# Kernel tuning notes

Measured on AMD Instinct MI355X. Metric: run time of the kernel, lower is better.

Reference implementation:

```python
import jax, jax.numpy as jnp
import numpy as np

EPS = 0.01
BETA = 0.8
GAMMA_A = 0.01
GAMMA_W = 0.01
ALPHA = 1.0
N_UNITS = 128

def setup_inputs() -> dict:
    key = jax.random.key(0)
    ks = jax.random.split(key, 7)
    B, T, D_in, C_out = 512, 1024, 64, 10
    return {
        "x": jax.random.normal(ks[0], (B, T, D_in), dtype=jnp.float32),
        "E_w": jax.random.normal(ks[1], (N_UNITS, D_in), dtype=jnp.float32) / np.sqrt(D_in),
        "E_b": jax.random.normal(ks[2], (N_UNITS,), dtype=jnp.float32) * 0.01,
        "B_p": jax.random.normal(ks[3], (N_UNITS, N_UNITS), dtype=jnp.float32) / N_UNITS,
        "C_p": jax.random.normal(ks[4], (N_UNITS, N_UNITS), dtype=jnp.float32) / N_UNITS,
        "D_w": jax.random.normal(ks[5], (C_out, N_UNITS), dtype=jnp.float32) / np.sqrt(N_UNITS),
        "D_b": jax.random.normal(ks[6], (C_out,), dtype=jnp.float32) * 0.01,
    }

def reference(x, E_w, E_b, B_p, C_p, D_w, D_b):
    B, T, _ = x.shape
    I = jnp.eye(N_UNITS, dtype=x.dtype)
    # Skew/symmetric mixture recurrent matrices (computed once, as in i==0 branch)
    A = BETA * (B_p - B_p.T) + (1.0 - BETA) * (B_p + B_p.T) - GAMMA_A * I
    W = BETA * (C_p - C_p.T) + (1.0 - BETA) * (C_p + C_p.T) - GAMMA_W * I
    # Input projection for all timesteps at once: [T, B, n_units]
    Z = jnp.einsum('bti,ui->tbu', x, E_w) + E_b
    h0 = jnp.zeros((B, N_UNITS), dtype=x.dtype)

    def step(h, z):
        h_update = ALPHA * (h @ A) + jnp.tanh(h @ W + z)
        return h + EPS * h_update, None

    h_final, _ = jax.lax.scan(step, h0, Z)
    return h_final @ D_w.T + D_b
```

## Files before the change

kernel.cpp:

```cpp
#include <hip/hip_runtime.h>

#define EPS_C 0.01f
#define NU    128
#define DIN   64
#define COUT  10

typedef float    f32x4 __attribute__((ext_vector_type(4)));
typedef _Float16 f16x4 __attribute__((ext_vector_type(4)));
typedef _Float16 f16x8 __attribute__((ext_vector_type(8)));

#define MFMA32(A, B, C) __builtin_amdgcn_mfma_f32_16x16x32_f16((A), (B), (C), 0, 0, 0)
#define BAR() asm volatile("s_waitcnt lgkmcnt(0)\n\ts_barrier" ::: "memory")

__global__ __launch_bounds__(256, 1)
void rnn_core(const float* __restrict__ x,
              const float* __restrict__ E_w, const float* __restrict__ E_b,
              const float* __restrict__ B_p, const float* __restrict__ C_p,
              const float* __restrict__ D_w, const float* __restrict__ D_b,
              float* __restrict__ out, int T)
{
    const int tid  = threadIdx.x;
    const int lane = tid & 63;
    const int w    = tid >> 6;
    const int lid  = lane & 15;
    const int q    = lane >> 4;
    const int g    = blockIdx.x;

    __shared__ __attribute__((aligned(16))) _Float16 xs[2][8 * 1024];
    __shared__ __attribute__((aligned(16))) _Float16 hbuf[2][4][64][8];
    __shared__ float hfin[16][NU + 4];

    f16x8 AT[2][4], WT[2][4], EF[2][2];
    f32x4 ebv[2];
    #pragma unroll
    for (int mt = 0; mt < 2; ++mt) {
        const int m = w * 32 + mt * 16 + lid;
        #pragma unroll
        for (int kt = 0; kt < 4; ++kt) {
            f16x8 fa, fw;
            #pragma unroll
            for (int j = 0; j < 8; ++j) {
                const int k  = kt * 32 + q * 8 + j;
                const float dg = (k == m) ? 0.01f : 0.0f;
                fa[j] = (_Float16)(B_p[k * NU + m] - 0.6f * B_p[m * NU + k] - dg);
                fw[j] = (_Float16)(C_p[k * NU + m] - 0.6f * C_p[m * NU + k] - dg);
            }
            AT[mt][kt] = fa;  WT[mt][kt] = fw;
        }
        #pragma unroll
        for (int kt = 0; kt < 2; ++kt) {
            f16x8 fe;
            #pragma unroll
            for (int j = 0; j < 8; ++j)
                fe[j] = (_Float16)E_w[m * DIN + kt * 32 + q * 8 + j];
            EF[mt][kt] = fe;
        }
        #pragma unroll
        for (int r = 0; r < 4; ++r)
            ebv[mt][r] = E_b[w * 32 + mt * 16 + q * 4 + r];
    }

    const int bb = tid & 15;
    const int s2 = tid >> 4;
    const float* xrow = x + ((size_t)(g * 16 + bb) * T) * DIN + s2 * 4;
    const int wb2 = (((s2 >> 3) * 64) + (((s2 >> 1) & 3) * 16) + bb) * 16 + (s2 & 1) * 8;

    float4 xg[8];

#define STAGE_WRITE(BUF)                                                      \
    {                                                                         \
        char* base_ = (char*)&xs[(BUF)][0];                                   \
        _Pragma("unroll")                                                     \
        for (int i2 = 0; i2 < 8; ++i2) {                                      \
            float4 v_ = xg[i2];                                               \
            f16x4 h4_;                                                        \
            h4_[0] = (_Float16)v_.x; h4_[1] = (_Float16)v_.y;                 \
            h4_[2] = (_Float16)v_.z; h4_[3] = (_Float16)v_.w;                 \
            *(f16x4*)(base_ + i2 * 2048 + wb2) = h4_;                         \
        }                                                                     \
    }

    ((float4*)&hbuf[0][0][0][0])[tid] = (float4){0.f, 0.f, 0.f, 0.f};
    #pragma unroll
    for (int i = 0; i < 8; ++i)
        xg[i] = *(const float4*)(xrow + (size_t)i * DIN);
    STAGE_WRITE(0)
    __syncthreads();

    char* xsb = (char*)&xs[0][0] + lane * 16;
    char* hrb = (char*)&hbuf[0][0][0][0] + lane * 16;
    char* hwb = (char*)&hbuf[0][0][0][0]
              + (w * 64 + (q >> 1) * 16 + lid) * 16 + (q & 1) * 8;

    f32x4 hf[2] = {{0.f,0.f,0.f,0.f}, {0.f,0.f,0.f,0.f}};
    f32x4 zc0, zc1;
    {
        f16x8 x0 = *(const f16x8*)(xsb);
        f16x8 x1 = *(const f16x8*)(xsb + 1024);
        zc0 = ebv[0];
        zc0 = MFMA32(EF[0][0], x0, zc0);
        zc0 = MFMA32(EF[0][1], x1, zc0);
        zc1 = ebv[1];
        zc1 = MFMA32(EF[1][0], x0, zc1);
        zc1 = MFMA32(EF[1][1], x1, zc1);
    }

    const int nch = T >> 3;
    for (int c = 0; c < nch; ++c) {
        if (c + 1 < nch) {
            const float* xr2 = xrow + (size_t)(c + 1) * 8 * DIN;
            #pragma unroll
            for (int i = 0; i < 8; ++i)
                xg[i] = *(const float4*)(xr2 + (size_t)i * DIN);
        }
        #pragma unroll
        for (int i = 0; i < 8; ++i) {
            const int t  = c * 8 + i;
            const int p  = i & 1;
            const int np = p ^ 1;

            f16x8 hB[4];
            #pragma unroll
            for (int kt = 0; kt < 4; ++kt)
                hB[kt] = *(const f16x8*)(hrb + p * 4096 + kt * 1024);

            int tt = t + 1; if (tt >= T) tt = T - 1;
            char* xb = xsb + ((tt >> 3) & 1) * 16384 + (tt & 7) * 2048;
            f16x8 xfA = *(const f16x8*)(xb);
            f16x8 xfB = *(const f16x8*)(xb + 1024);

            f32x4 wa0 = zc0, wa1 = zc1;
            #pragma unroll
            for (int kt = 0; kt < 4; ++kt) {
                wa0 = MFMA32(WT[0][kt], hB[kt], wa0);
                wa1 = MFMA32(WT[1][kt], hB[kt], wa1);
            }
            f32x4 ya0 = {0.f,0.f,0.f,0.f}, ya1 = {0.f,0.f,0.f,0.f};
            #pragma unroll
            for (int kt = 0; kt < 4; ++kt) {
                ya0 = MFMA32(AT[0][kt], hB[kt], ya0);
                ya1 = MFMA32(AT[1][kt], hB[kt], ya1);
            }
            f32x4 zn0 = ebv[0], zn1 = ebv[1];
            zn0 = MFMA32(EF[0][0], xfA, zn0);
            zn1 = MFMA32(EF[1][0], xfA, zn1);
            zn0 = MFMA32(EF[0][1], xfB, zn0);
            zn1 = MFMA32(EF[1][1], xfB, zn1);

            #pragma unroll
            for (int mt = 0; mt < 2; ++mt) {
                f32x4 wa = mt ? wa1 : wa0;
                f32x4 ya = mt ? ya1 : ya0;
                f16x4 nh;
                #pragma unroll
                for (int r = 0; r < 4; ++r) {
                    const float e2 = __builtin_amdgcn_exp2f(wa[r] * 2.8853900817779268f);
                    const float th = 1.0f - 2.0f * __builtin_amdgcn_rcpf(e2 + 1.0f);
                    const float hv = hf[mt][r] + EPS_C * (ya[r] + th);
                    hf[mt][r] = hv;
                    nh[r] = (_Float16)hv;
                }
                *(f16x4*)(hwb + np * 4096 + mt * 512) = nh;
            }
            zc0 = zn0; zc1 = zn1;

            if (i == 5 && c + 1 < nch) STAGE_WRITE((c + 1) & 1)
            BAR();
        }
    }

    #pragma unroll
    for (int mt = 0; mt < 2; ++mt)
        #pragma unroll
        for (int r = 0; r < 4; ++r)
            hfin[lid][w * 32 + mt * 16 + q * 4 + r] = hf[mt][r];
    __syncthreads();

    if (tid < 16 * COUT) {
        const int r  = tid / COUT;
        const int cc = tid - r * COUT;
        float acc = D_b[cc];
        #pragma unroll 8
        for (int u = 0; u < NU; ++u)
            acc = fmaf(hfin[r][u], D_w[cc * NU + u], acc);
        out[((size_t)g * 16 + r) * COUT + cc] = acc;
    }
}

extern "C" void kernel_launch(void* const* d_in, const int* in_sizes, int n_in,
                              void* d_out, int out_size, void* d_ws, size_t ws_size,
                              hipStream_t stream)
{
    const float* x   = (const float*)d_in[0];
    const float* E_w = (const float*)d_in[1];
    const float* E_b = (const float*)d_in[2];
    const float* B_p = (const float*)d_in[3];
    const float* C_p = (const float*)d_in[4];
    const float* D_w = (const float*)d_in[5];
    const float* D_b = (const float*)d_in[6];
    float* out = (float*)d_out;

    const int B  = out_size / COUT;
    const int T  = in_sizes[0] / (B * DIN);
    const int NB = B / 16;

    rnn_core<<<NB, 256, 0, stream>>>(x, E_w, E_b, B_p, C_p, D_w, D_b, out, T);
}
```

Before: 588.1 us.

## Process two independent 16-row batch groups per block to interleave recurrence chains

Each block now handles 32 batch rows as two independent groups that share the register-resident recurrent and input-projection weight fragments. The MFMA chains and tanh updates of the two groups are interleaved within each timestep so one group's work can fill the other's latency, and the per-step barrier is shared. The x staging for the second group is spread across different substeps. This halves the grid size, leaving more CUs idle and doubling per-step work and register pressure per block.

```diff
diff --git a/kernel.cpp b/kernel.cpp
--- a/kernel.cpp
+++ b/kernel.cpp
@@ -26,9 +26,9 @@
     const int q    = lane >> 4;
     const int g    = blockIdx.x;
 
-    __shared__ __attribute__((aligned(16))) _Float16 xs[2][8 * 1024];
-    __shared__ __attribute__((aligned(16))) _Float16 hbuf[2][4][64][8];
-    __shared__ float hfin[16][NU + 4];
+    __shared__ __attribute__((aligned(16))) _Float16 xs[2][2][8192];
+    __shared__ __attribute__((aligned(16))) _Float16 hbuf[2][2][4][64][8];
+    __shared__ float hfin[32][NU + 4];
 
     f16x8 AT[2][4], WT[2][4], EF[2][2];
     f32x4 ebv[2];
@@ -62,14 +62,15 @@
 
     const int bb = tid & 15;
     const int s2 = tid >> 4;
-    const float* xrow = x + ((size_t)(g * 16 + bb) * T) * DIN + s2 * 4;
+    const float* xrow0 = x + ((size_t)(g * 32 + bb) * T) * DIN + s2 * 4;
+    const float* xrow1 = xrow0 + (size_t)16 * T * DIN;
     const int wb2 = (((s2 >> 3) * 64) + (((s2 >> 1) & 3) * 16) + bb) * 16 + (s2 & 1) * 8;
 
     float4 xg[8];
 
-#define STAGE_WRITE(BUF)                                                      \
+#define STAGE_WRITE(GR, BUF)                                                  \
     {                                                                         \
-        char* base_ = (char*)&xs[(BUF)][0];                                   \
+        char* base_ = (char*)xs + (GR) * 32768 + (BUF) * 16384;               \
         _Pragma("unroll")                                                     \
         for (int i2 = 0; i2 < 8; ++i2) {                                      \
             float4 v_ = xg[i2];                                               \
@@ -80,110 +81,151 @@
         }                                                                     \
     }
 
-    ((float4*)&hbuf[0][0][0][0])[tid] = (float4){0.f, 0.f, 0.f, 0.f};
+    #pragma unroll
+    for (int k2 = 0; k2 < 4; ++k2)
+        ((float4*)hbuf)[k2 * 256 + tid] = (float4){0.f, 0.f, 0.f, 0.f};
     #pragma unroll
     for (int i = 0; i < 8; ++i)
-        xg[i] = *(const float4*)(xrow + (size_t)i * DIN);
-    STAGE_WRITE(0)
+        xg[i] = *(const float4*)(xrow0 + (size_t)i * DIN);
+    STAGE_WRITE(0, 0)
+    #pragma unroll
+    for (int i = 0; i < 8; ++i)
+        xg[i] = *(const float4*)(xrow1 + (size_t)i * DIN);
+    STAGE_WRITE(1, 0)
     __syncthreads();
 
-    char* xsb = (char*)&xs[0][0] + lane * 16;
-    char* hrb = (char*)&hbuf[0][0][0][0] + lane * 16;
-    char* hwb = (char*)&hbuf[0][0][0][0]
+    char* xsb = (char*)xs + lane * 16;
+    char* hrb = (char*)hbuf + lane * 16;
+    char* hwb = (char*)hbuf
               + (w * 64 + (q >> 1) * 16 + lid) * 16 + (q & 1) * 8;
 
-    f32x4 hf[2] = {{0.f,0.f,0.f,0.f}, {0.f,0.f,0.f,0.f}};
-    f32x4 zc0, zc1;
-    {
-        f16x8 x0 = *(const f16x8*)(xsb);
-        f16x8 x1 = *(const f16x8*)(xsb + 1024);
-        zc0 = ebv[0];
-        zc0 = MFMA32(EF[0][0], x0, zc0);
-        zc0 = MFMA32(EF[0][1], x1, zc0);
-        zc1 = ebv[1];
-        zc1 = MFMA32(EF[1][0], x0, zc1);
-        zc1 = MFMA32(EF[1][1], x1, zc1);
+    f32x4 hf[2][2] = {{{0.f,0.f,0.f,0.f},{0.f,0.f,0.f,0.f}},
+                      {{0.f,0.f,0.f,0.f},{0.f,0.f,0.f,0.f}}};
+    f32x4 zc[2][2];
+    #pragma unroll
+    for (int gr = 0; gr < 2; ++gr) {
+        f16x8 xa = *(const f16x8*)(xsb + gr * 32768);
+        f16x8 xb = *(const f16x8*)(xsb + gr * 32768 + 1024);
+        #pragma unroll
+        for (int mt = 0; mt < 2; ++mt) {
+            f32x4 z = ebv[mt];
+            z = MFMA32(EF[mt][0], xa, z);
+            z = MFMA32(EF[mt][1], xb, z);
+            zc[gr][mt] = z;
+        }
     }
 
     const int nch = T >> 3;
     for (int c = 0; c < nch; ++c) {
-        if (c + 1 < nch) {
-            const float* xr2 = xrow + (size_t)(c + 1) * 8 * DIN;
-            #pragma unroll
-            for (int i = 0; i < 8; ++i)
-                xg[i] = *(const float4*)(xr2 + (size_t)i * DIN);
-        }
         #pragma unroll
         for (int i = 0; i < 8; ++i) {
             const int t  = c * 8 + i;
             const int p  = i & 1;
             const int np = p ^ 1;
 
-            f16x8 hB[4];
+            if (i == 0 && c + 1 < nch) {
+                const float* xr = xrow0 + (size_t)(c + 1) * 8 * DIN;
+                #pragma unroll
+                for (int k = 0; k < 8; ++k)
+                    xg[k] = *(const float4*)(xr + (size_t)k * DIN);
+            }
+
+            f16x8 hB[2][4];
+            #pragma unroll
+            for (int gr = 0; gr < 2; ++gr)
+                #pragma unroll
+                for (int kt = 0; kt < 4; ++kt)
+                    hB[gr][kt] = *(const f16x8*)(hrb + gr * 8192 + p * 4096 + kt * 1024);
+
+            int tt = t + 1; if (tt >= T) tt = T - 1;
+            const int xoff = ((tt >> 3) & 1) * 16384 + (tt & 7) * 2048;
+            f16x8 xf[2][2];
+            #pragma unroll
+            for (int gr = 0; gr < 2; ++gr) {
+                xf[gr][0] = *(const f16x8*)(xsb + gr * 32768 + xoff);
+                xf[gr][1] = *(const f16x8*)(xsb + gr * 32768 + xoff + 1024);
+            }
+
+            f32x4 wa[2][2], ya[2][2], zn[2][2];
+            #pragma unroll
+            for (int gr = 0; gr < 2; ++gr) {
+                wa[gr][0] = zc[gr][0]; wa[gr][1] = zc[gr][1];
+            }
             #pragma unroll
             for (int kt = 0; kt < 4; ++kt)
-                hB[kt] = *(const f16x8*)(hrb + p * 4096 + kt * 1024);
-
-            int tt = t + 1; if (tt >= T) tt = T - 1;
-            char* xb = xsb + ((tt >> 3) & 1) * 16384 + (tt & 7) * 2048;
-            f16x8 xfA = *(const f16x8*)(xb);
-            f16x8 xfB = *(const f16x8*)(xb + 1024);
-
-            f32x4 wa0 = zc0, wa1 = zc1;
-            #pragma unroll
-            for (int kt = 0; kt < 4; ++kt) {
-                wa0 = MFMA32(WT[0][kt], hB[kt], wa0);
-                wa1 = MFMA32(WT[1][kt], hB[kt], wa1);
-            }
-            f32x4 ya0 = {0.f,0.f,0.f,0.f}, ya1 = {0.f,0.f,0.f,0.f};
-            #pragma unroll
-            for (int kt = 0; kt < 4; ++kt) {
-                ya0 = MFMA32(AT[0][kt], hB[kt], ya0);
-                ya1 = MFMA32(AT[1][kt], hB[kt], ya1);
-            }
-            f32x4 zn0 = ebv[0], zn1 = ebv[1];
-            zn0 = MFMA32(EF[0][0], xfA, zn0);
-            zn1 = MFMA32(EF[1][0], xfA, zn1);
-            zn0 = MFMA32(EF[0][1], xfB, zn0);
-            zn1 = MFMA32(EF[1][1], xfB, zn1);
-
-            #pragma unroll
-            for (int mt = 0; mt < 2; ++mt) {
-                f32x4 wa = mt ? wa1 : wa0;
-                f32x4 ya = mt ? ya1 : ya0;
-                f16x4 nh;
-                #pragma unroll
-                for (int r = 0; r < 4; ++r) {
-                    const float e2 = __builtin_amdgcn_exp2f(wa[r] * 2.8853900817779268f);
-                    const float th = 1.0f - 2.0f * __builtin_amdgcn_rcpf(e2 + 1.0f);
-                    const float hv = hf[mt][r] + EPS_C * (ya[r] + th);
-                    hf[mt][r] = hv;
-                    nh[r] = (_Float16)hv;
+                #pragma unroll
+                for (int gr = 0; gr < 2; ++gr) {
+                    wa[gr][0] = MFMA32(WT[0][kt], hB[gr][kt], wa[gr][0]);
+                    wa[gr][1] = MFMA32(WT[1][kt], hB[gr][kt], wa[gr][1]);
                 }
-                *(f16x4*)(hwb + np * 4096 + mt * 512) = nh;
-            }
-            zc0 = zn0; zc1 = zn1;
-
-            if (i == 5 && c + 1 < nch) STAGE_WRITE((c + 1) & 1)
+            #pragma unroll
+            for (int gr = 0; gr < 2; ++gr) {
+                ya[gr][0] = (f32x4){0.f,0.f,0.f,0.f};
+                ya[gr][1] = (f32x4){0.f,0.f,0.f,0.f};
+            }
+            #pragma unroll
+            for (int kt = 0; kt < 4; ++kt)
+                #pragma unroll
+                for (int gr = 0; gr < 2; ++gr) {
+                    ya[gr][0] = MFMA32(AT[0][kt], hB[gr][kt], ya[gr][0]);
+                    ya[gr][1] = MFMA32(AT[1][kt], hB[gr][kt], ya[gr][1]);
+                }
+            #pragma unroll
+            for (int gr = 0; gr < 2; ++gr) {
+                zn[gr][0] = ebv[0]; zn[gr][1] = ebv[1];
+                zn[gr][0] = MFMA32(EF[0][0], xf[gr][0], zn[gr][0]);
+                zn[gr][1] = MFMA32(EF[1][0], xf[gr][0], zn[gr][1]);
+                zn[gr][0] = MFMA32(EF[0][1], xf[gr][1], zn[gr][0]);
+                zn[gr][1] = MFMA32(EF[1][1], xf[gr][1], zn[gr][1]);
+            }
+
+            #pragma unroll
+            for (int gr = 0; gr < 2; ++gr) {
+                #pragma unroll
+                for (int mt = 0; mt < 2; ++mt) {
+                    f16x4 nh;
+                    #pragma unroll
+                    for (int r = 0; r < 4; ++r) {
+                        const float e2 = __builtin_amdgcn_exp2f(wa[gr][mt][r] * 2.8853900817779268f);
+                        const float th = 1.0f - 2.0f * __builtin_amdgcn_rcpf(e2 + 1.0f);
+                        const float hv = hf[gr][mt][r] + EPS_C * (ya[gr][mt][r] + th);
+                        hf[gr][mt][r] = hv;
+                        nh[r] = (_Float16)hv;
+                    }
+                    *(f16x4*)(hwb + gr * 8192 + np * 4096 + mt * 512) = nh;
+                }
+                zc[gr][0] = zn[gr][0]; zc[gr][1] = zn[gr][1];
+            }
+
+            if (i == 3 && c + 1 < nch) {
+                STAGE_WRITE(0, (c + 1) & 1)
+                const float* xr = xrow1 + (size_t)(c + 1) * 8 * DIN;
+                #pragma unroll
+                for (int k = 0; k < 8; ++k)
+                    xg[k] = *(const float4*)(xr + (size_t)k * DIN);
+            }
+            if (i == 6 && c + 1 < nch) STAGE_WRITE(1, (c + 1) & 1)
             BAR();
         }
     }
 
     #pragma unroll
-    for (int mt = 0; mt < 2; ++mt)
-        #pragma unroll
-        for (int r = 0; r < 4; ++r)
-            hfin[lid][w * 32 + mt * 16 + q * 4 + r] = hf[mt][r];
+    for (int gr = 0; gr < 2; ++gr)
+        #pragma unroll
+        for (int mt = 0; mt < 2; ++mt)
+            #pragma unroll
+            for (int r = 0; r < 4; ++r)
+                hfin[gr * 16 + lid][w * 32 + mt * 16 + q * 4 + r] = hf[gr][mt][r];
     __syncthreads();
 
-    if (tid < 16 * COUT) {
-        const int r  = tid / COUT;
-        const int cc = tid - r * COUT;
+    for (int idx = tid; idx < 32 * COUT; idx += 256) {
+        const int r  = idx / COUT;
+        const int cc = idx - r * COUT;
         float acc = D_b[cc];
         #pragma unroll 8
         for (int u = 0; u < NU; ++u)
             acc = fmaf(hfin[r][u], D_w[cc * NU + u], acc);
-        out[((size_t)g * 16 + r) * COUT + cc] = acc;
+        out[((size_t)g * 32 + r) * COUT + cc] = acc;
     }
 }
 
@@ -202,7 +244,7 @@
 
     const int B  = out_size / COUT;
     const int T  = in_sizes[0] / (B * DIN);
-    const int NB = B / 16;
+    const int NB = B / 32;
 
     rnn_core<<<NB, 256, 0, stream>>>(x, E_w, E_b, B_p, C_p, D_w, D_b, out, T);
 }
```

Result: slower. 954.5 us (+62.3%).

## Precompute input projection in separate kernel and stream Z from workspace

Applied to the files above, without the earlier changes.

Adds a fully parallel pre-kernel that computes Z = x·E_wᵀ + E_b for all timesteps into the workspace as fp32. The recurrent kernel then loads Z from global memory with a two-step prefetch instead of staging x through LDS and running four extra MFMAs per step. The aim is to shorten the serial per-step chain, at the cost of a large intermediate buffer (about 256 MB write plus read) and global-load latency on the critical path. The original fused kernel is kept as a fallback when the workspace is too small.

```diff
diff --git a/kernel.cpp b/kernel.cpp
--- a/kernel.cpp
+++ b/kernel.cpp
@@ -13,11 +13,71 @@
 #define BAR() asm volatile("s_waitcnt lgkmcnt(0)\n\ts_barrier" ::: "memory")
 
 __global__ __launch_bounds__(256, 1)
-void rnn_core(const float* __restrict__ x,
-              const float* __restrict__ E_w, const float* __restrict__ E_b,
-              const float* __restrict__ B_p, const float* __restrict__ C_p,
-              const float* __restrict__ D_w, const float* __restrict__ D_b,
-              float* __restrict__ out, int T)
+void z_pre(const float* __restrict__ x, const float* __restrict__ E_w,
+           const float* __restrict__ E_b, float* __restrict__ zf, int T)
+{
+    const int tid  = threadIdx.x;
+    const int lane = tid & 63;
+    const int w    = tid >> 6;
+    const int lid  = lane & 15;
+    const int q    = lane >> 4;
+    const int tc   = blockIdx.x;
+    const int g    = blockIdx.y;
+
+    __shared__ __attribute__((aligned(16))) _Float16 xs[8192];
+
+    f16x8 EF[2][2];
+    f32x4 ebv[2];
+    #pragma unroll
+    for (int mt = 0; mt < 2; ++mt) {
+        const int m = w * 32 + mt * 16 + lid;
+        #pragma unroll
+        for (int kt = 0; kt < 2; ++kt) {
+            f16x8 fe;
+            #pragma unroll
+            for (int j = 0; j < 8; ++j)
+                fe[j] = (_Float16)E_w[m * DIN + kt * 32 + q * 8 + j];
+            EF[mt][kt] = fe;
+        }
+        #pragma unroll
+        for (int r = 0; r < 4; ++r)
+            ebv[mt][r] = E_b[w * 32 + mt * 16 + q * 4 + r];
+    }
+
+    const int bb = tid & 15;
+    const int s2 = tid >> 4;
+    const float* xrow = x + ((size_t)(g * 16 + bb) * T + (size_t)tc * 8) * DIN + s2 * 4;
+    const int wb2 = (((s2 >> 3) * 64) + (((s2 >> 1) & 3) * 16) + bb) * 16 + (s2 & 1) * 8;
+    #pragma unroll
+    for (int i = 0; i < 8; ++i) {
+        float4 v = *(const float4*)(xrow + (size_t)i * DIN);
+        f16x4 h4;
+        h4[0] = (_Float16)v.x; h4[1] = (_Float16)v.y;
+        h4[2] = (_Float16)v.z; h4[3] = (_Float16)v.w;
+        *(f16x4*)((char*)xs + i * 2048 + wb2) = h4;
+    }
+    __syncthreads();
+
+    const char* xsb = (const char*)xs + lane * 16;
+    float* zd = zf + ((size_t)g * T + (size_t)tc * 8) * 2048 + w * 512 + q * 64 + lid * 4;
+    #pragma unroll
+    for (int i = 0; i < 8; ++i) {
+        f16x8 x0 = *(const f16x8*)(xsb + i * 2048);
+        f16x8 x1 = *(const f16x8*)(xsb + i * 2048 + 1024);
+        #pragma unroll
+        for (int mt = 0; mt < 2; ++mt) {
+            f32x4 z = ebv[mt];
+            z = MFMA32(EF[mt][0], x0, z);
+            z = MFMA32(EF[mt][1], x1, z);
+            *(f32x4*)(zd + (size_t)i * 2048 + mt * 256) = z;
+        }
+    }
+}
+
+__global__ __launch_bounds__(256, 1)
+void rnn_core_z(const float* __restrict__ B_p, const float* __restrict__ C_p,
+                const float* __restrict__ D_w, const float* __restrict__ D_b,
+                const float* __restrict__ zf, float* __restrict__ out, int T)
 {
     const int tid  = threadIdx.x;
     const int lane = tid & 63;
@@ -26,12 +86,10 @@
     const int q    = lane >> 4;
     const int g    = blockIdx.x;
 
-    __shared__ __attribute__((aligned(16))) _Float16 xs[2][8 * 1024];
     __shared__ __attribute__((aligned(16))) _Float16 hbuf[2][4][64][8];
     __shared__ float hfin[16][NU + 4];
 
-    f16x8 AT[2][4], WT[2][4], EF[2][2];
-    f32x4 ebv[2];
+    f16x8 AT[2][4], WT[2][4];
     #pragma unroll
     for (int mt = 0; mt < 2; ++mt) {
         const int m = w * 32 + mt * 16 + lid;
@@ -47,75 +105,29 @@
             }
             AT[mt][kt] = fa;  WT[mt][kt] = fw;
         }
-        #pragma unroll
-        for (int kt = 0; kt < 2; ++kt) {
-            f16x8 fe;
-            #pragma unroll
-            for (int j = 0; j < 8; ++j)
-                fe[j] = (_Float16)E_w[m * DIN + kt * 32 + q * 8 + j];
-            EF[mt][kt] = fe;
-        }
-        #pragma unroll
-        for (int r = 0; r < 4; ++r)
-            ebv[mt][r] = E_b[w * 32 + mt * 16 + q * 4 + r];
-    }
-
-    const int bb = tid & 15;
-    const int s2 = tid >> 4;
-    const float* xrow = x + ((size_t)(g * 16 + bb) * T) * DIN + s2 * 4;
-    const int wb2 = (((s2 >> 3) * 64) + (((s2 >> 1) & 3) * 16) + bb) * 16 + (s2 & 1) * 8;
-
-    float4 xg[8];
-
-#define STAGE_WRITE(BUF)                                                      \
-    {                                                                         \
-        char* base_ = (char*)&xs[(BUF)][0];                                   \
-        _Pragma("unroll")                                                     \
-        for (int i2 = 0; i2 < 8; ++i2) {                                      \
-            float4 v_ = xg[i2];                                               \
-            f16x4 h4_;                                                        \
-            h4_[0] = (_Float16)v_.x; h4_[1] = (_Float16)v_.y;                 \
-            h4_[2] = (_Float16)v_.z; h4_[3] = (_Float16)v_.w;                 \
-            *(f16x4*)(base_ + i2 * 2048 + wb2) = h4_;                         \
-        }                                                                     \
     }
 
     ((float4*)&hbuf[0][0][0][0])[tid] = (float4){0.f, 0.f, 0.f, 0.f};
-    #pragma unroll
-    for (int i = 0; i < 8; ++i)
-        xg[i] = *(const float4*)(xrow + (size_t)i * DIN);
-    STAGE_WRITE(0)
-    __syncthreads();
-
-    char* xsb = (char*)&xs[0][0] + lane * 16;
-    char* hrb = (char*)&hbuf[0][0][0][0] + lane * 16;
-    char* hwb = (char*)&hbuf[0][0][0][0]
+    __syncthreads();
+
+    char* hrb = (char*)hbuf + lane * 16;
+    char* hwb = (char*)hbuf
               + (w * 64 + (q >> 1) * 16 + lid) * 16 + (q & 1) * 8;
 
+    const float* zbase = zf + (size_t)g * T * 2048 + w * 512 + q * 64 + lid * 4;
+#define ZLD(T_, MT_) (*(const f32x4*)(zbase + (size_t)(T_) * 2048 + (MT_) * 256))
+
     f32x4 hf[2] = {{0.f,0.f,0.f,0.f}, {0.f,0.f,0.f,0.f}};
-    f32x4 zc0, zc1;
-    {
-        f16x8 x0 = *(const f16x8*)(xsb);
-        f16x8 x1 = *(const f16x8*)(xsb + 1024);
-        zc0 = ebv[0];
-        zc0 = MFMA32(EF[0][0], x0, zc0);
-        zc0 = MFMA32(EF[0][1], x1, zc0);
-        zc1 = ebv[1];
-        zc1 = MFMA32(EF[1][0], x0, zc1);
-        zc1 = MFMA32(EF[1][1], x1, zc1);
-    }
+    f32x4 zs[2][2];
+    zs[0][0] = ZLD(0, 0);  zs[0][1] = ZLD(0, 1);
+    zs[1][0] = ZLD(1, 0);  zs[1][1] = ZLD(1, 1);
 
     const int nch = T >> 3;
     for (int c = 0; c < nch; ++c) {
-        if (c + 1 < nch) {
-            const float* xr2 = xrow + (size_t)(c + 1) * 8 * DIN;
-            #pragma unroll
-            for (int i = 0; i < 8; ++i)
-                xg[i] = *(const float4*)(xr2 + (size_t)i * DIN);
-        }
         #pragma unroll
         for (int i = 0; i < 8; ++i) {
             const int t  = c * 8 + i;
+            const int sl = i & 1;
             const int p  = i & 1;
             const int np = p ^ 1;
 
@@ -124,12 +136,7 @@
             for (int kt = 0; kt < 4; ++kt)
                 hB[kt] = *(const f16x8*)(hrb + p * 4096 + kt * 1024);
 
-            int tt = t + 1; if (tt >= T) tt = T - 1;
-            char* xb = xsb + ((tt >> 3) & 1) * 16384 + (tt & 7) * 2048;
-            f16x8 xfA = *(const f16x8*)(xb);
-            f16x8 xfB = *(const f16x8*)(xb + 1024);
-
-            f32x4 wa0 = zc0, wa1 = zc1;
+            f32x4 wa0 = zs[sl][0], wa1 = zs[sl][1];
             #pragma unroll
             for (int kt = 0; kt < 4; ++kt) {
                 wa0 = MFMA32(WT[0][kt], hB[kt], wa0);
@@ -141,11 +148,12 @@
                 ya0 = MFMA32(AT[0][kt], hB[kt], ya0);
                 ya1 = MFMA32(AT[1][kt], hB[kt], ya1);
             }
-            f32x4 zn0 = ebv[0], zn1 = ebv[1];
-            zn0 = MFMA32(EF[0][0], xfA, zn0);
-            zn1 = MFMA32(EF[1][0], xfA, zn1);
-            zn0 = MFMA32(EF[0][1], xfB, zn0);
-            zn1 = MFMA32(EF[1][1], xfB, zn1);
+
+            {
+                int t2 = t + 2; if (t2 >= T) t2 = T - 1;
+                zs[sl][0] = ZLD(t2, 0);
+                zs[sl][1] = ZLD(t2, 1);
+            }
 
             #pragma unroll
             for (int mt = 0; mt < 2; ++mt) {
@@ -162,9 +170,183 @@
                 }
                 *(f16x4*)(hwb + np * 4096 + mt * 512) = nh;
             }
+
+            BAR();
+        }
+    }
+
+    #pragma unroll
+    for (int mt = 0; mt < 2; ++mt)
+        #pragma unroll
+        for (int r = 0; r < 4; ++r)
+            hfin[lid][w * 32 + mt * 16 + q * 4 + r] = hf[mt][r];
+    __syncthreads();
+
+    if (tid < 16 * COUT) {
+        const int r  = tid / COUT;
+        const int cc = tid - r * COUT;
+        float acc = D_b[cc];
+        #pragma unroll 8
+        for (int u = 0; u < NU; ++u)
+            acc = fmaf(hfin[r][u], D_w[cc * NU + u], acc);
+        out[((size_t)g * 16 + r) * COUT + cc] = acc;
+    }
+}
+
+__global__ __launch_bounds__(256, 1)
+void rnn_core_v1(const float* __restrict__ x,
+                 const float* __restrict__ E_w, const float* __restrict__ E_b,
+                 const float* __restrict__ B_p, const float* __restrict__ C_p,
+                 const float* __restrict__ D_w, const float* __restrict__ D_b,
+                 float* __restrict__ out, int T)
+{
+    const int tid  = threadIdx.x;
+    const int lane = tid & 63;
+    const int w    = tid >> 6;
+    const int lid  = lane & 15;
+    const int q    = lane >> 4;
+    const int g    = blockIdx.x;
+
+    __shared__ __attribute__((aligned(16))) _Float16 xs[2][8 * 1024];
+    __shared__ __attribute__((aligned(16))) _Float16 hbuf[2][4][64][8];
+    __shared__ float hfin[16][NU + 4];
+
+    f16x8 AT[2][4], WT[2][4], EF[2][2];
+    f32x4 ebv[2];
+    #pragma unroll
+    for (int mt = 0; mt < 2; ++mt) {
+        const int m = w * 32 + mt * 16 + lid;
+        #pragma unroll
+        for (int kt = 0; kt < 4; ++kt) {
+            f16x8 fa, fw;
+            #pragma unroll
+            for (int j = 0; j < 8; ++j) {
+                const int k  = kt * 32 + q * 8 + j;
+                const float dg = (k == m) ? 0.01f : 0.0f;
+                fa[j] = (_Float16)(B_p[k * NU + m] - 0.6f * B_p[m * NU + k] - dg);
+                fw[j] = (_Float16)(C_p[k * NU + m] - 0.6f * C_p[m * NU + k] - dg);
+            }
+            AT[mt][kt] = fa;  WT[mt][kt] = fw;
+        }
+        #pragma unroll
+        for (int kt = 0; kt < 2; ++kt) {
+            f16x8 fe;
+            #pragma unroll
+            for (int j = 0; j < 8; ++j)
+                fe[j] = (_Float16)E_w[m * DIN + kt * 32 + q * 8 + j];
+            EF[mt][kt] = fe;
+        }
+        #pragma unroll
+        for (int r = 0; r < 4; ++r)
+            ebv[mt][r] = E_b[w * 32 + mt * 16 + q * 4 + r];
+    }
+
+    const int bb = tid & 15;
+    const int s2 = tid >> 4;
+    const float* xrow = x + ((size_t)(g * 16 + bb) * T) * DIN + s2 * 4;
+    const int wb2 = (((s2 >> 3) * 64) + (((s2 >> 1) & 3) * 16) + bb) * 16 + (s2 & 1) * 8;
+
+    float4 xg[8];
+
+#define STAGE_WRITE_V1(BUF)                                                   \
+    {                                                                         \
+        char* base_ = (char*)&xs[(BUF)][0];                                   \
+        _Pragma("unroll")                                                     \
+        for (int i2 = 0; i2 < 8; ++i2) {                                      \
+            float4 v_ = xg[i2];                                               \
+            f16x4 h4_;                                                        \
+            h4_[0] = (_Float16)v_.x; h4_[1] = (_Float16)v_.y;                 \
+            h4_[2] = (_Float16)v_.z; h4_[3] = (_Float16)v_.w;                 \
+            *(f16x4*)(base_ + i2 * 2048 + wb2) = h4_;                         \
+        }                                                                     \
+    }
+
+    ((float4*)&hbuf[0][0][0][0])[tid] = (float4){0.f, 0.f, 0.f, 0.f};
+    #pragma unroll
+    for (int i = 0; i < 8; ++i)
+        xg[i] = *(const float4*)(xrow + (size_t)i * DIN);
+    STAGE_WRITE_V1(0)
+    __syncthreads();
+
+    char* xsb = (char*)&xs[0][0] + lane * 16;
+    char* hrb = (char*)&hbuf[0][0][0][0] + lane * 16;
+    char* hwb = (char*)&hbuf[0][0][0][0]
+              + (w * 64 + (q >> 1) * 16 + lid) * 16 + (q & 1) * 8;
+
+    f32x4 hf[2] = {{0.f,0.f,0.f,0.f}, {0.f,0.f,0.f,0.f}};
+    f32x4 zc0, zc1;
+    {
+        f16x8 x0 = *(const f16x8*)(xsb);
+        f16x8 x1 = *(const f16x8*)(xsb + 1024);
+        zc0 = ebv[0];
+        zc0 = MFMA32(EF[0][0], x0, zc0);
+        zc0 = MFMA32(EF[0][1], x1, zc0);
+        zc1 = ebv[1];
+        zc1 = MFMA32(EF[1][0], x0, zc1);
+        zc1 = MFMA32(EF[1][1], x1, zc1);
+    }
+
+    const int nch = T >> 3;
+    for (int c = 0; c < nch; ++c) {
+        if (c + 1 < nch) {
+            const float* xr2 = xrow + (size_t)(c + 1) * 8 * DIN;
+            #pragma unroll
+            for (int i = 0; i < 8; ++i)
+                xg[i] = *(const float4*)(xr2 + (size_t)i * DIN);
+        }
+        #pragma unroll
+        for (int i = 0; i < 8; ++i) {
+            const int t  = c * 8 + i;
+            const int p  = i & 1;
+            const int np = p ^ 1;
+
+            f16x8 hB[4];
+            #pragma unroll
+            for (int kt = 0; kt < 4; ++kt)
+                hB[kt] = *(const f16x8*)(hrb + p * 4096 + kt * 1024);
+
+            int tt = t + 1; if (tt >= T) tt = T - 1;
+            const int it = tt & 7;
+            char* xb = xsb + ((tt >> 3) & 1) * 16384 + it * 2048;
+            f16x8 xfA = *(const f16x8*)(xb);
+            f16x8 xfB = *(const f16x8*)(xb + 1024);
+
+            f32x4 wa0 = zc0, wa1 = zc1;
+            #pragma unroll
+            for (int kt = 0; kt < 4; ++kt) {
+                wa0 = MFMA32(WT[0][kt], hB[kt], wa0);
+                wa1 = MFMA32(WT[1][kt], hB[kt], wa1);
+            }
+            f32x4 ya0 = {0.f,0.f,0.f,0.f}, ya1 = {0.f,0.f,0.f,0.f};
+            #pragma unroll
+            for (int kt = 0; kt < 4; ++kt) {
+                ya0 = MFMA32(AT[0][kt], hB[kt], ya0);
+                ya1 = MFMA32(AT[1][kt], hB[kt], ya1);
+            }
+            f32x4 zn0 = ebv[0], zn1 = ebv[1];
+            zn0 = MFMA32(EF[0][0], xfA, zn0);
+            zn1 = MFMA32(EF[1][0], xfA, zn1);
+            zn0 = MFMA32(EF[0][1], xfB, zn0);
+            zn1 = MFMA32(EF[1][1], xfB, zn1);
+
+            #pragma unroll
+            for (int mt = 0; mt < 2; ++mt) {
+                f32x4 wa = mt ? wa1 : wa0;
+                f32x4 ya = mt ? ya1 : ya0;
+                f16x4 nh;
+                #pragma unroll
+                for (int r = 0; r < 4; ++r) {
+                    const float e2 = __builtin_amdgcn_exp2f(wa[r] * 2.8853900817779268f);
+                    const float th = 1.0f - 2.0f * __builtin_amdgcn_rcpf(e2 + 1.0f);
+                    const float hv = hf[mt][r] + EPS_C * (ya[r] + th);
+                    hf[mt][r] = hv;
+                    nh[r] = (_Float16)hv;
+                }
+                *(f16x4*)(hwb + np * 4096 + mt * 512) = nh;
+            }
             zc0 = zn0; zc1 = zn1;
 
-            if (i == 5 && c + 1 < nch) STAGE_WRITE((c + 1) & 1)
+            if (i == 5 && c + 1 < nch) STAGE_WRITE_V1((c + 1) & 1)
             BAR();
         }
     }
@@ -202,7 +384,14 @@
 
     const int B  = out_size / COUT;
     const int T  = in_sizes[0] / (B * DIN);
-    const int NB = B / 16;
-
-    rnn_core<<<NB, 256, 0, stream>>>(x, E_w, E_b, B_p, C_p, D_w, D_b, out, T);
+    const int NG = B / 16;
+
+    const size_t zbytes = (size_t)NG * T * 2048 * sizeof(float);
+    if (d_ws && ws_size >= zbytes && (T & 7) == 0) {
+        float* zf = (float*)d_ws;
+        z_pre<<<dim3(T / 8, NG), 256, 0, stream>>>(x, E_w, E_b, zf, T);
+        rnn_core_z<<<NG, 256, 0, stream>>>(B_p, C_p, D_w, D_b, zf, out, T);
+    } else {
+        rnn_core_v1<<<NG, 256, 0, stream>>>(x, E_w, E_b, B_p, C_p, D_w, D_b, out, T);
+    }
 }
```

After: 677.6 us. 1.15x slower.

## Fold tanh scale into weights and accumulate A·h directly into scaled state

Applied to the files above, without the earlier changes.

The 2/ln2 tanh argument scale is folded into the W, E and bias tensors at load time, so the exp2 input needs no multiply. The recurrent state is now kept as h/EPS, and the A·h MFMA chain accumulates straight into it, which removes the separate ya accumulator and the per-element scale-and-add. exp2 and rcp are issued before the A MFMAs so they can overlap with them. The fp16 conversion now uses packed round-toward-zero, which slightly changes rounding of the shared hidden state.

```diff
diff --git a/kernel.cpp b/kernel.cpp
--- a/kernel.cpp
+++ b/kernel.cpp
@@ -4,8 +4,10 @@
 #define NU    128
 #define DIN   64
 #define COUT  10
+#define TSCALE 2.8853900817779268f
 
 typedef float    f32x4 __attribute__((ext_vector_type(4)));
+typedef _Float16 f16x2 __attribute__((ext_vector_type(2)));
 typedef _Float16 f16x4 __attribute__((ext_vector_type(4)));
 typedef _Float16 f16x8 __attribute__((ext_vector_type(8)));
 
@@ -43,7 +45,7 @@
                 const int k  = kt * 32 + q * 8 + j;
                 const float dg = (k == m) ? 0.01f : 0.0f;
                 fa[j] = (_Float16)(B_p[k * NU + m] - 0.6f * B_p[m * NU + k] - dg);
-                fw[j] = (_Float16)(C_p[k * NU + m] - 0.6f * C_p[m * NU + k] - dg);
+                fw[j] = (_Float16)((C_p[k * NU + m] - 0.6f * C_p[m * NU + k] - dg) * TSCALE);
             }
             AT[mt][kt] = fa;  WT[mt][kt] = fw;
         }
@@ -52,12 +54,12 @@
             f16x8 fe;
             #pragma unroll
             for (int j = 0; j < 8; ++j)
-                fe[j] = (_Float16)E_w[m * DIN + kt * 32 + q * 8 + j];
+                fe[j] = (_Float16)(E_w[m * DIN + kt * 32 + q * 8 + j] * TSCALE);
             EF[mt][kt] = fe;
         }
         #pragma unroll
         for (int r = 0; r < 4; ++r)
-            ebv[mt][r] = E_b[w * 32 + mt * 16 + q * 4 + r];
+            ebv[mt][r] = E_b[w * 32 + mt * 16 + q * 4 + r] * TSCALE;
     }
 
     const int bb = tid & 15;
@@ -135,11 +137,18 @@
                 wa0 = MFMA32(WT[0][kt], hB[kt], wa0);
                 wa1 = MFMA32(WT[1][kt], hB[kt], wa1);
             }
-            f32x4 ya0 = {0.f,0.f,0.f,0.f}, ya1 = {0.f,0.f,0.f,0.f};
+
+            float rc[2][4];
+            #pragma unroll
+            for (int r = 0; r < 4; ++r) {
+                rc[0][r] = __builtin_amdgcn_rcpf(__builtin_amdgcn_exp2f(wa0[r]) + 1.0f);
+                rc[1][r] = __builtin_amdgcn_rcpf(__builtin_amdgcn_exp2f(wa1[r]) + 1.0f);
+            }
+
             #pragma unroll
             for (int kt = 0; kt < 4; ++kt) {
-                ya0 = MFMA32(AT[0][kt], hB[kt], ya0);
-                ya1 = MFMA32(AT[1][kt], hB[kt], ya1);
+                hf[0] = MFMA32(AT[0][kt], hB[kt], hf[0]);
+                hf[1] = MFMA32(AT[1][kt], hB[kt], hf[1]);
             }
             f32x4 zn0 = ebv[0], zn1 = ebv[1];
             zn0 = MFMA32(EF[0][0], xfA, zn0);
@@ -149,17 +158,15 @@
 
             #pragma unroll
             for (int mt = 0; mt < 2; ++mt) {
-                f32x4 wa = mt ? wa1 : wa0;
-                f32x4 ya = mt ? ya1 : ya0;
+                #pragma unroll
+                for (int r = 0; r < 4; ++r)
+                    hf[mt][r] = __builtin_fmaf(-2.0f, rc[mt][r], hf[mt][r] + 1.0f);
+                f16x2 lo = __builtin_bit_cast(f16x2,
+                    __builtin_amdgcn_cvt_pkrtz(EPS_C * hf[mt][0], EPS_C * hf[mt][1]));
+                f16x2 hi = __builtin_bit_cast(f16x2,
+                    __builtin_amdgcn_cvt_pkrtz(EPS_C * hf[mt][2], EPS_C * hf[mt][3]));
                 f16x4 nh;
-                #pragma unroll
-                for (int r = 0; r < 4; ++r) {
-                    const float e2 = __builtin_amdgcn_exp2f(wa[r] * 2.8853900817779268f);
-                    const float th = 1.0f - 2.0f * __builtin_amdgcn_rcpf(e2 + 1.0f);
-                    const float hv = hf[mt][r] + EPS_C * (ya[r] + th);
-                    hf[mt][r] = hv;
-                    nh[r] = (_Float16)hv;
-                }
+                nh[0] = lo[0]; nh[1] = lo[1]; nh[2] = hi[0]; nh[3] = hi[1];
                 *(f16x4*)(hwb + np * 4096 + mt * 512) = nh;
             }
             zc0 = zn0; zc1 = zn1;
@@ -173,7 +180,7 @@
     for (int mt = 0; mt < 2; ++mt)
         #pragma unroll
         for (int r = 0; r < 4; ++r)
-            hfin[lid][w * 32 + mt * 16 + q * 4 + r] = hf[mt][r];
+            hfin[lid][w * 32 + mt * 16 + q * 4 + r] = EPS_C * hf[mt][r];
     __syncthreads();
 
     if (tid < 16 * COUT) {
```

Result: no change. 586.9 us (-0.2%).
